# Kernel tuning notes

Measured on AMD Instinct MI355X. Metric: run time of the kernel, lower is better.

## Reference

```python
import jax, jax.numpy as jnp
import numpy as np

D_MODEL = 1024
D_HIDDEN = 16384
N_TOKENS = 8192
K = 32


def setup_inputs() -> dict:
    key = jax.random.key(0)
    k1, k2, k3 = jax.random.split(key, 3)
    x = jax.random.normal(k1, (N_TOKENS, D_MODEL), dtype=jnp.float32)
    # encoder.weight: [d_hidden, d_model] (torch Linear convention)
    W_enc = jax.random.normal(k2, (D_HIDDEN, D_MODEL), dtype=jnp.float32) * (1.0 / np.sqrt(D_MODEL))
    # decoder.weight: [d_model, d_hidden], column-normalized as in __init__
    W_dec = jax.random.normal(k3, (D_MODEL, D_HIDDEN), dtype=jnp.float32)
    W_dec = W_dec / (jnp.linalg.norm(W_dec, axis=0, keepdims=True) + 1e-8)
    b_pre = jnp.zeros((D_MODEL,), dtype=jnp.float32)
    b_act = jnp.zeros((D_HIDDEN,), dtype=jnp.float32)
    return {"x": x, "W_enc": W_enc, "W_dec": W_dec, "b_pre": b_pre, "b_act": b_act, "k": K}


def reference(x, W_enc, W_dec, b_pre, b_act, k):
    # encode
    x_cent = x - b_pre                                   # [N, d_model]
    pre_acts = jnp.einsum('nd,hd->nh', x_cent, W_enc) + b_act  # [N, d_hidden]
    # top-k hard activation with straight-through estimator
    vals, inds = jax.lax.top_k(pre_acts, k)              # [N, k]
    rows = jnp.arange(pre_acts.shape[0])[:, None]        # [N, 1]
    hard = jnp.zeros_like(pre_acts).at[rows, inds].set(jax.nn.relu(vals))
    sparse_acts = hard + (pre_acts - jax.lax.stop_gradient(pre_acts))
    # decode
    recon = jnp.einsum('nh,dh->nd', sparse_acts, W_dec) + b_pre  # [N, d_model]
    return (recon, sparse_acts, pre_acts)
```

## Files before the change

kernel.cpp:

```cpp
#include <hip/hip_runtime.h>
#include <hip/hip_bf16.h>

#define N_TOK   8192
#define DM      1024
#define DH      16384
#define KTOP    32
#define NCAND   256

typedef unsigned int uint;
typedef __attribute__((ext_vector_type(8))) short bf16x8;
typedef __attribute__((ext_vector_type(4))) float f32x4;

__device__ inline ushort f2bf(float f) {
    uint u = __float_as_uint(f);
    uint r = (u + 0x7FFFu + ((u >> 16) & 1u)) >> 16;
    return (ushort)r;
}
__device__ inline float bf2f(ushort u) {
    return __uint_as_float(((uint)u) << 16);
}

__device__ inline void load_lds16(const void* g, void* l) {
    __builtin_amdgcn_global_load_lds(
        (const __attribute__((address_space(1))) void*)g,
        (__attribute__((address_space(3))) void*)l, 16, 0, 0);
}

__global__ __launch_bounds__(256) void conv_x(
    const float* __restrict__ x, const float* __restrict__ b_pre,
    ushort* __restrict__ A)
{
    int i = (blockIdx.x * 256 + threadIdx.x) * 4;
    float4 v = *(const float4*)&x[i];
    float4 b = *(const float4*)&b_pre[i & (DM - 1)];
    ushort4 o;
    o.x = f2bf(v.x - b.x); o.y = f2bf(v.y - b.y);
    o.z = f2bf(v.z - b.z); o.w = f2bf(v.w - b.w);
    *(ushort4*)&A[i] = o;
}

__global__ __launch_bounds__(256) void conv_w(
    const float* __restrict__ W, ushort* __restrict__ B)
{
    int i = (blockIdx.x * 256 + threadIdx.x) * 4;
    float4 v = *(const float4*)&W[i];
    ushort4 o;
    o.x = f2bf(v.x); o.y = f2bf(v.y); o.z = f2bf(v.z); o.w = f2bf(v.w);
    *(ushort4*)&B[i] = o;
}

__global__ __launch_bounds__(256, 3) void gemm_bf16(
    const ushort* __restrict__ A, const ushort* __restrict__ B,
    const float* __restrict__ b_act, float* __restrict__ pre)
{
    __shared__ ushort As[128 * 64];
    __shared__ ushort Bs[128 * 64];

    const int tid  = threadIdx.x;
    const int wid  = tid >> 6;
    const int lane = tid & 63;
    const int wr   = wid >> 1;
    const int wc   = wid & 1;

    int swz = (blockIdx.x & 7) * 1024 + (blockIdx.x >> 3);
    const int bm = swz & 63;
    const int bn = swz >> 6;
    const int row0 = bm * 128;
    const int col0 = bn * 128;

    f32x4 acc[4][4] = {};

    const int chunk = wid * 64 + lane;
    for (int k0 = 0; k0 < DM; k0 += 64) {
        #pragma unroll
        for (int i = 0; i < 4; ++i) {
            int ch = i * 256 + chunk;
            int r  = ch >> 3;
            int c8 = (ch & 7) * 8;
            load_lds16(&A[(size_t)(row0 + r) * DM + k0 + c8],
                       &As[(size_t)(i * 256 + wid * 64) * 8]);
            load_lds16(&B[(size_t)(col0 + r) * DM + k0 + c8],
                       &Bs[(size_t)(i * 256 + wid * 64) * 8]);
        }
        __syncthreads();
        #pragma unroll
        for (int ks = 0; ks < 2; ++ks) {
            const int kb = ks * 32 + (lane >> 4) * 8;
            bf16x8 af[4], bfr[4];
            #pragma unroll
            for (int m = 0; m < 4; ++m)
                af[m] = *(const bf16x8*)&As[(wr * 64 + m * 16 + (lane & 15)) * 64 + kb];
            #pragma unroll
            for (int n = 0; n < 4; ++n)
                bfr[n] = *(const bf16x8*)&Bs[(wc * 64 + n * 16 + (lane & 15)) * 64 + kb];
            #pragma unroll
            for (int m = 0; m < 4; ++m)
                #pragma unroll
                for (int n = 0; n < 4; ++n)
                    acc[m][n] = __builtin_amdgcn_mfma_f32_16x16x32_bf16(
                        af[m], bfr[n], acc[m][n], 0, 0, 0);
        }
        __syncthreads();
    }

    const int ccol = col0 + wc * 64 + (lane & 15);
    float ba[4];
    #pragma unroll
    for (int n = 0; n < 4; ++n) ba[n] = b_act[ccol + n * 16];
    #pragma unroll
    for (int m = 0; m < 4; ++m) {
        const int crow = row0 + wr * 64 + m * 16 + (lane >> 4) * 4;
        #pragma unroll
        for (int r = 0; r < 4; ++r) {
            #pragma unroll
            for (int n = 0; n < 4; ++n)
                pre[(size_t)(crow + r) * DH + ccol + n * 16] = acc[m][n][r] + ba[n];
        }
    }
}

__global__ __launch_bounds__(512) void topk_cand(
    const float* __restrict__ pre, float* __restrict__ sparse,
    float* __restrict__ cval, int* __restrict__ cidx, int* __restrict__ ccnt)
{
    const int row = blockIdx.x;
    const int tid = threadIdx.x;
    const float* __restrict__ p = pre + (size_t)row * DH;

    float v[32];
    #pragma unroll
    for (int j = 0; j < 32; ++j) v[j] = p[j * 512 + tid];

    float4 z = {0.f, 0.f, 0.f, 0.f};
    float4* srow = (float4*)(sparse + (size_t)row * DH);
    #pragma unroll
    for (int i = 0; i < 8; ++i) srow[tid + i * 512] = z;

    __shared__ int scount;
    float lo = -30.f, hi = 30.f, t = 0.f;
    for (int it = 0; it < 20; ++it) {
        t = 0.5f * (lo + hi);
        int c = 0;
        #pragma unroll
        for (int j = 0; j < 32; ++j) c += (v[j] > t);
        #pragma unroll
        for (int off = 32; off; off >>= 1) c += __shfl_down(c, off);
        if (tid == 0) scount = 0;
        __syncthreads();
        if ((tid & 63) == 0) atomicAdd(&scount, c);
        __syncthreads();
        int total = scount;
        __syncthreads();
        if (total >= 96 && total <= 250) break;
        if (total < 96) hi = t; else lo = t;
    }

    __shared__ int wpos;
    __shared__ float scv[NCAND];
    __shared__ int   sci[NCAND];
    if (tid == 0) wpos = 0;
    __syncthreads();
    #pragma unroll
    for (int j = 0; j < 32; ++j) {
        if (v[j] > t) {
            int pz = atomicAdd(&wpos, 1);
            if (pz < NCAND) { scv[pz] = v[j]; sci[pz] = j * 512 + tid; }
        }
    }
    __syncthreads();
    int n = min(wpos, NCAND);
    if (tid == 0) ccnt[row] = n;
    if (tid < NCAND) {
        cval[(size_t)row * NCAND + tid] = (tid < n) ? scv[tid] : -1e30f;
        cidx[(size_t)row * NCAND + tid] = (tid < n) ? sci[tid] : -1;
    }
}

__device__ inline void bitonic256(float* key, float* val, int* idx, int tid)
{
    for (int k = 2; k <= 256; k <<= 1) {
        for (int j = k >> 1; j; j >>= 1) {
            int ixj = tid ^ j;
            if (ixj > tid) {
                float ka = key[tid], kb = key[ixj];
                int ia = idx[tid], ib = idx[ixj];
                bool a_first = (ka > kb) || (ka == kb && ia < ib);
                bool desc = ((tid & k) == 0);
                if (desc != a_first) {
                    key[tid] = kb; key[ixj] = ka;
                    float va = val[tid]; val[tid] = val[ixj]; val[ixj] = va;
                    idx[tid] = ib; idx[ixj] = ia;
                }
            }
            __syncthreads();
        }
    }
}

__global__ __launch_bounds__(256) void fix_topk(
    const float* __restrict__ x, const float* __restrict__ b_pre,
    const float* __restrict__ W, const float* __restrict__ b_act,
    const float* __restrict__ cval, const int* __restrict__ cidx,
    float* __restrict__ sparse, float* __restrict__ vals, int* __restrict__ inds)
{
    const int row = blockIdx.x;
    const int tid = threadIdx.x;
    const int wid = tid >> 6, lane = tid & 63;

    __shared__ float xs[DM];
    for (int i = tid; i < DM; i += 256)
        xs[i] = x[(size_t)row * DM + i] - b_pre[i];

    __shared__ float key[NCAND];
    __shared__ float val[NCAND];
    __shared__ int   idx[NCAND];
    key[tid] = cval[(size_t)row * NCAND + tid];
    val[tid] = key[tid];
    idx[tid] = cidx[(size_t)row * NCAND + tid];
    __syncthreads();

    bitonic256(key, val, idx, tid);

    const float DZ = 0.04f;
    float a32 = key[31];
    __shared__ int z0s, z1s;
    if (tid == 0) { z0s = 256; z1s = 256; }
    __syncthreads();
    if (key[tid] <= a32 + DZ) atomicMin(&z0s, tid);
    if (key[tid] <  a32 - DZ) atomicMin(&z1s, tid);
    __syncthreads();
    const int z0 = z0s, z1 = z1s;

    for (int m = z0 + wid; m < z1; m += 4) {
        int h = idx[m];
        if (h >= 0) {
            const float* wrow = W + (size_t)h * DM;
            float s = 0.f;
            #pragma unroll
            for (int c = 0; c < 16; ++c)
                s = fmaf(xs[lane + c * 64], wrow[lane + c * 64], s);
            #pragma unroll
            for (int off = 32; off; off >>= 1) s += __shfl_down(s, off);
            if (lane == 0) { float e = s + b_act[h]; key[m] = e; val[m] = e; }
        }
    }
    __syncthreads();

    if (tid < z0)       key[tid] = 1e30f - (float)tid;
    else if (tid >= z1) key[tid] = -1e30f;
    __syncthreads();

    bitonic256(key, val, idx, tid);

    if (tid < KTOP) {
        float v = val[tid];
        int h = idx[tid];
        float r = v > 0.f ? v : 0.f;
        vals[(size_t)row * KTOP + tid] = r;
        inds[(size_t)row * KTOP + tid] = h;
        if (h >= 0) sparse[(size_t)row * DH + h] = r;
    }
}

__global__ __launch_bounds__(256) void transpose_dec(
    const float* __restrict__ W, ushort* __restrict__ WT)
{
    __shared__ float t[32][33];
    const int tx = threadIdx.x;
    const int ty = threadIdx.y;
    const int h0 = blockIdx.x * 32;
    const int d0 = blockIdx.y * 32;
    #pragma unroll
    for (int r = 0; r < 4; ++r)
        t[ty + r * 8][tx] = W[(size_t)(d0 + ty + r * 8) * DH + h0 + tx];
    __syncthreads();
    #pragma unroll
    for (int r = 0; r < 4; ++r)
        WT[(size_t)(h0 + ty + r * 8) * DM + d0 + tx] = f2bf(t[tx][ty + r * 8]);
}

__global__ __launch_bounds__(256) void recon_kernel(
    const float* __restrict__ vals, const int* __restrict__ inds,
    const ushort* __restrict__ wdecT, const float* __restrict__ b_pre,
    float* __restrict__ recon)
{
    const int row = blockIdx.x;
    const int tid = threadIdx.x;
    __shared__ float lval[KTOP];
    __shared__ int   lind[KTOP];
    if (tid < KTOP) {
        lval[tid] = vals[(size_t)row * KTOP + tid];
        lind[tid] = inds[(size_t)row * KTOP + tid];
    }
    __syncthreads();

    const int d = tid * 4;
    float4 a = *(const float4*)&b_pre[d];
    #pragma unroll 8
    for (int j = 0; j < KTOP; ++j) {
        float vj = lval[j];
        int h = lind[j];
        if (vj != 0.f && h >= 0) {
            ushort4 w = *(const ushort4*)&wdecT[(size_t)h * DM + d];
            a.x = fmaf(vj, bf2f(w.x), a.x);
            a.y = fmaf(vj, bf2f(w.y), a.y);
            a.z = fmaf(vj, bf2f(w.z), a.z);
            a.w = fmaf(vj, bf2f(w.w), a.w);
        }
    }
    *(float4*)&recon[(size_t)row * DM + d] = a;
}

extern "C" void kernel_launch(void* const* d_in, const int* in_sizes, int n_in,
                              void* d_out, int out_size, void* d_ws, size_t ws_size,
                              hipStream_t stream)
{
    const float* x     = (const float*)d_in[0];
    const float* W_enc = (const float*)d_in[1];
    const float* W_dec = (const float*)d_in[2];
    const float* b_pre = (const float*)d_in[3];
    const float* b_act = (const float*)d_in[4];

    float* recon  = (float*)d_out;
    float* sparse = recon + (size_t)N_TOK * DM;
    float* pre    = sparse + (size_t)N_TOK * DH;

    ushort* Abf = (ushort*)sparse;
    ushort* Bbf = Abf + (size_t)N_TOK * DM;

    float*  cval  = (float*)d_ws;
    int*    cidx  = (int*)(cval + (size_t)N_TOK * NCAND);
    int*    ccnt  = cidx + (size_t)N_TOK * NCAND;
    float*  vals  = (float*)(ccnt + N_TOK);
    int*    inds  = (int*)(vals + (size_t)N_TOK * KTOP);
    ushort* wdecT = (ushort*)(inds + (size_t)N_TOK * KTOP);

    conv_x<<<N_TOK * DM / 1024, 256, 0, stream>>>(x, b_pre, Abf);
    conv_w<<<DH * DM / 1024, 256, 0, stream>>>(W_enc, Bbf);

    gemm_bf16<<<(N_TOK / 128) * (DH / 128), 256, 0, stream>>>(Abf, Bbf, b_act, pre);

    transpose_dec<<<dim3(DH / 32, DM / 32), dim3(32, 8), 0, stream>>>(W_dec, wdecT);

    topk_cand<<<N_TOK, 512, 0, stream>>>(pre, sparse, cval, cidx, ccnt);

    fix_topk<<<N_TOK, 256, 0, stream>>>(x, b_pre, W_enc, b_act,
                                        cval, cidx, sparse, vals, inds);

    recon_kernel<<<N_TOK, 256, 0, stream>>>(vals, inds, wdecT, b_pre, recon);
}
```

Measured before the change: 910.7 us.

## Replace bitonic sorts in top-k fixup with rank counting and zone recompute

```diff
diff --git a/kernel.cpp b/kernel.cpp
--- a/kernel.cpp
+++ b/kernel.cpp
@@ -6,6 +6,7 @@
 #define DH      16384
 #define KTOP    32
 #define NCAND   256
+#define DZ      0.08f
 
 typedef unsigned int uint;
 typedef __attribute__((ext_vector_type(8))) short bf16x8;
@@ -176,27 +177,6 @@
     }
 }
 
-__device__ inline void bitonic256(float* key, float* val, int* idx, int tid)
-{
-    for (int k = 2; k <= 256; k <<= 1) {
-        for (int j = k >> 1; j; j >>= 1) {
-            int ixj = tid ^ j;
-            if (ixj > tid) {
-                float ka = key[tid], kb = key[ixj];
-                int ia = idx[tid], ib = idx[ixj];
-                bool a_first = (ka > kb) || (ka == kb && ia < ib);
-                bool desc = ((tid & k) == 0);
-                if (desc != a_first) {
-                    key[tid] = kb; key[ixj] = ka;
-                    float va = val[tid]; val[tid] = val[ixj]; val[ixj] = va;
-                    idx[tid] = ib; idx[ixj] = ia;
-                }
-            }
-            __syncthreads();
-        }
-    }
-}
-
 __global__ __launch_bounds__(256) void fix_topk(
     const float* __restrict__ x, const float* __restrict__ b_pre,
     const float* __restrict__ W, const float* __restrict__ b_act,
@@ -211,54 +191,78 @@
     for (int i = tid; i < DM; i += 256)
         xs[i] = x[(size_t)row * DM + i] - b_pre[i];
 
-    __shared__ float key[NCAND];
-    __shared__ float val[NCAND];
-    __shared__ int   idx[NCAND];
-    key[tid] = cval[(size_t)row * NCAND + tid];
-    val[tid] = key[tid];
-    idx[tid] = cidx[(size_t)row * NCAND + tid];
-    __syncthreads();
-
-    bitonic256(key, val, idx, tid);
-
-    const float DZ = 0.04f;
-    float a32 = key[31];
-    __shared__ int z0s, z1s;
-    if (tid == 0) { z0s = 256; z1s = 256; }
-    __syncthreads();
-    if (key[tid] <= a32 + DZ) atomicMin(&z0s, tid);
-    if (key[tid] <  a32 - DZ) atomicMin(&z1s, tid);
-    __syncthreads();
-    const int z0 = z0s, z1 = z1s;
-
-    for (int m = z0 + wid; m < z1; m += 4) {
-        int h = idx[m];
-        if (h >= 0) {
-            const float* wrow = W + (size_t)h * DM;
-            float s = 0.f;
-            #pragma unroll
-            for (int c = 0; c < 16; ++c)
-                s = fmaf(xs[lane + c * 64], wrow[lane + c * 64], s);
-            #pragma unroll
-            for (int off = 32; off; off >>= 1) s += __shfl_down(s, off);
-            if (lane == 0) { float e = s + b_act[h]; key[m] = e; val[m] = e; }
-        }
-    }
-    __syncthreads();
-
-    if (tid < z0)       key[tid] = 1e30f - (float)tid;
-    else if (tid >= z1) key[tid] = -1e30f;
-    __syncthreads();
-
-    bitonic256(key, val, idx, tid);
-
+    __shared__ float sv[NCAND];
+    __shared__ float sex[NCAND];
+    __shared__ int   si[NCAND];
+    __shared__ int   zlist[NCAND];
+    __shared__ unsigned char zf[NCAND];
+    __shared__ float sa32;
+    __shared__ int   scin, zn;
+
+    const float v  = cval[(size_t)row * NCAND + tid];
+    const int   id = cidx[(size_t)row * NCAND + tid];
+    sv[tid] = v; si[tid] = id; sex[tid] = v;
+    if (tid == 0) { scin = 0; zn = 0; }
     if (tid < KTOP) {
-        float v = val[tid];
-        int h = idx[tid];
-        float r = v > 0.f ? v : 0.f;
-        vals[(size_t)row * KTOP + tid] = r;
-        inds[(size_t)row * KTOP + tid] = h;
-        if (h >= 0) sparse[(size_t)row * DH + h] = r;
+        vals[(size_t)row * KTOP + tid] = 0.f;
+        inds[(size_t)row * KTOP + tid] = -1;
+    }
+    __syncthreads();
+
+    int rank = 0;
+    for (int j = 0; j < NCAND; ++j) {
+        float ov = sv[j];
+        rank += (ov > v) || (ov == v && si[j] < id);
+    }
+    if (rank == 31) sa32 = v;
+    __syncthreads();
+
+    const float a32 = sa32;
+    const bool cin  = v > a32 + DZ;
+    const bool zone = !cin && (v >= a32 - DZ) && (id >= 0);
+
+    unsigned long long bal = __ballot(cin);
+    if (lane == 0) atomicAdd(&scin, (int)__popcll(bal));
+    if (zone) { int p = atomicAdd(&zn, 1); zlist[p] = tid; }
+    zf[tid] = zone ? 1 : 0;
+    __syncthreads();
+
+    const int cin_total = scin;
+    const int znum = zn;
+
+    for (int m = wid; m < znum; m += 4) {
+        int t = zlist[m];
+        int h = si[t];
+        const float* wrow = W + (size_t)h * DM;
+        float s = 0.f;
+        #pragma unroll
+        for (int c = 0; c < 16; ++c)
+            s = fmaf(xs[lane + c * 64], wrow[lane + c * 64], s);
+        #pragma unroll
+        for (int off = 32; off; off >>= 1) s += __shfl_down(s, off);
+        if (lane == 0) sex[t] = s + b_act[h];
+    }
+    __syncthreads();
+
+    int slot = -1;
+    float outv = 0.f;
+    if (cin) { slot = rank; outv = v; }
+    else if (zone) {
+        float ev = sex[tid];
+        int zrank = 0;
+        for (int j = 0; j < NCAND; ++j) {
+            if (zf[j]) {
+                float ov = sex[j];
+                zrank += (ov > ev) || (ov == ev && si[j] < id);
+            }
+        }
+        if (zrank < KTOP - cin_total) { slot = cin_total + zrank; outv = ev; }
+    }
+    if (slot >= 0) {
+        float r = fmaxf(outv, 0.f);
+        vals[(size_t)row * KTOP + slot] = r;
+        inds[(size_t)row * KTOP + slot] = id;
+        sparse[(size_t)row * DH + id] = r;
     }
 }
 
```

Result: no change. 920.0 us (+1.0%).
